# Kernel tuning notes

Measured on AMD Instinct MI355X. Metric: run time of the kernel, lower is better.

The kernel has to match this reference:

```python
import jax, jax.numpy as jnp
import numpy as np

N_NODES = 50000


def setup_inputs() -> dict:
    key = jax.random.key(0)
    k1, k2, k3, k4 = jax.random.split(key, 4)
    in_dim, out_dim, n_edges = 128, 64, 800000
    x = jax.random.normal(k1, (N_NODES, in_dim), dtype=jnp.float32)
    edge_index = jax.random.randint(k2, (2, n_edges), 0, N_NODES, dtype=jnp.int64)
    W = jax.random.normal(k3, (in_dim, out_dim), dtype=jnp.float32) * (1.0 / np.sqrt(in_dim))
    att = jax.random.normal(k4, (2 * out_dim,), dtype=jnp.float32) * (1.0 / np.sqrt(2 * out_dim))
    return {"x": x, "edge_index": edge_index, "W": W, "att": att}


def reference(x, edge_index, W, att):
    N = x.shape[0]
    F_out = W.shape[1]
    h = x @ W                                   # [N, F]
    src, dst = edge_index[0], edge_index[1]
    hs = h[src]                                 # [E, F] gather
    hd = h[dst]                                 # [E, F] gather
    # att(cat([h_src, h_dst])) == h_src @ a1 + h_dst @ a2
    a1, a2 = att[:F_out], att[F_out:]
    logit = jax.nn.leaky_relu(hs @ a1 + hd @ a2, 0.2)   # [E]
    E = logit.shape[0]
    # The original builds a dense [N, E] matrix (row d holds logit_e at col e
    # for dst[e]==d, zeros elsewhere) and softmaxes over the E axis. The
    # equivalent sparse form: denom_d = sum_{e:dst=d} exp(logit_e) + (E - deg_d)*exp(0),
    # stabilized with m_d = max(max logit over segment, 0).
    seg_max = jax.ops.segment_max(logit, dst, num_segments=N)      # -inf on empty
    m = jnp.maximum(seg_max, 0.0)                                  # include the zero cells
    exp_l = jnp.exp(logit - m[dst])                                # [E]
    seg_sum = jax.ops.segment_sum(exp_l, dst, num_segments=N)      # [N]
    deg = jax.ops.segment_sum(jnp.ones_like(logit), dst, num_segments=N)
    denom = seg_sum + (jnp.float32(E) - deg) * jnp.exp(-m)         # zeros' contribution
    w = exp_l / denom[dst]                                          # [E]
    agg = jax.ops.segment_sum(w[:, None] * hs, dst, num_segments=N)  # [N, F]
    return jax.nn.elu(agg)
```

## Files before the change

### kernel.cpp

```cpp
#include <hip/hip_runtime.h>
#include <hip/hip_bf16.h>

#define FIN 128
#define FOUT 64
#define BINW 128
#define NBINPAD 512
#define QS 2560
#define TILE 4096
#define DPQ 32
#define RCAP 768

typedef __attribute__((ext_vector_type(8))) short short8;
typedef __attribute__((ext_vector_type(4))) float f32x4;

__device__ __forceinline__ unsigned short f2bf(float f) {
    unsigned u = __float_as_uint(f);
    unsigned r = u + 0x7FFFu + ((u >> 16) & 1u);
    return (unsigned short)(r >> 16);
}

__device__ __forceinline__ float f16lo(unsigned u) {
    return (float)__builtin_bit_cast(_Float16, (unsigned short)(u & 0xFFFFu));
}
__device__ __forceinline__ float f16hi(unsigned u) {
    return (float)__builtin_bit_cast(_Float16, (unsigned short)(u >> 16));
}

__global__ __launch_bounds__(256) void k_prep(
    const float* __restrict__ W,
    unsigned short* __restrict__ Whig, unsigned short* __restrict__ Wlog,
    int* __restrict__ qcur, int nzero)
{
    const int t = threadIdx.x;
    if (blockIdx.x >= 64) {
        const int i = (blockIdx.x - 64) * 256 + t;
        if (i < nzero) qcur[i] = 0;
        return;
    }
    const int f = blockIdx.x * 256 + t;
    const int combo = f >> 9;
    const int s = combo >> 2, c = combo & 3;
    const int r = f & 511;
    const int l = r >> 3, j = r & 7;
    const int k = s * 32 + (l >> 4) * 8 + j;
    const int n = c * 16 + (l & 15);
    const float w = W[k * 64 + n];
    const unsigned short hi = f2bf(w);
    const float hif = __uint_as_float((unsigned)hi << 16);
    Whig[f] = hi;
    Wlog[f] = f2bf(w - hif);
}

__global__ __launch_bounds__(256, 8) void k_fused(
    const float* __restrict__ x, const unsigned short* __restrict__ Whig,
    const unsigned short* __restrict__ Wlog, const float* __restrict__ att,
    unsigned* __restrict__ h2, float* __restrict__ as_, float* __restrict__ ad_,
    const int* __restrict__ src, const int* __restrict__ dst,
    unsigned* __restrict__ queue, int* __restrict__ qcur,
    int N, int E, int nbins, int paBlocks)
{
    union SMem {
        struct { unsigned rec[TILE]; int hist[NBINPAD]; int scanb[NBINPAD];
                 int comb[NBINPAD]; } pa;
    };
    __shared__ SMem sm;
    const int t = threadIdx.x;

    if ((int)blockIdx.x < paBlocks) {
        const int e0 = blockIdx.x * TILE;
        const int tot = (E - e0 < TILE) ? (E - e0) : TILE;
        sm.pa.hist[t] = 0; sm.pa.hist[t + 256] = 0;
        __syncthreads();
        #pragma unroll
        for (int i = 0; i < TILE / 256; ++i) {
            const int e = e0 + i * 256 + t;
            if (e < E) atomicAdd(&sm.pa.hist[__builtin_nontemporal_load(dst + e) >> 7], 1);
        }
        __syncthreads();
        const int v0 = sm.pa.hist[t], v1 = sm.pa.hist[t + 256];
        sm.pa.scanb[t] = v0; sm.pa.scanb[t + 256] = v1;
        __syncthreads();
        #pragma unroll
        for (int off = 1; off < NBINPAD; off <<= 1) {
            const int a0 = (t >= off) ? sm.pa.scanb[t - off] : 0;
            const int a1 = (t + 256 >= off) ? sm.pa.scanb[t + 256 - off] : 0;
            __syncthreads();
            sm.pa.scanb[t] += a0; sm.pa.scanb[t + 256] += a1;
            __syncthreads();
        }
        const int ex0 = sm.pa.scanb[t] - v0;
        const int ex1 = sm.pa.scanb[t + 256] - v1;
        int c0 = 0, c1 = 0;
        if (t < nbins && v0 > 0)
            c0 = t * QS + atomicAdd(qcur + t, v0) - ex0;
        if (t + 256 < nbins && v1 > 0)
            c1 = (t + 256) * QS + atomicAdd(qcur + t + 256, v1) - ex1;
        sm.pa.hist[t] = ex0; sm.pa.hist[t + 256] = ex1;
        sm.pa.comb[t] = c0;  sm.pa.comb[t + 256] = c1;
        __syncthreads();
        #pragma unroll
        for (int i = 0; i < TILE / 256; ++i) {
            const int e = e0 + i * 256 + t;
            if (e < E) {
                const int d = __builtin_nontemporal_load(dst + e);
                const int s = __builtin_nontemporal_load(src + e);
                const int pos = atomicAdd(&sm.pa.hist[d >> 7], 1);
                sm.pa.rec[pos] = (unsigned)s | ((unsigned)d << 16);
            }
        }
        __syncthreads();
        for (int i = t; i < tot; i += 256) {
            const unsigned r = sm.pa.rec[i];
            const int b = (int)(r >> 23);
            const int gpos = sm.pa.comb[b] + i;
            if (gpos < (b + 1) * QS)
                __builtin_nontemporal_store(r, queue + gpos);
        }
        return;
    }

    const int bb = blockIdx.x - paBlocks;
    const int wv = t >> 6, lane = t & 63;
    const int quad = lane >> 4, mrow = lane & 15;
    const int r0 = (bb * 4 + wv) * 16;
    const int arow = r0 + mrow;
    const bool rok = arow < N;

    f32x4 acc[4] = {};

    #pragma unroll
    for (int s = 0; s < 4; ++s) {
        float xv[8];
        if (rok) {
            const float4* p = (const float4*)(x + (size_t)arow * FIN + s * 32 + quad * 8);
            const float4 u0 = p[0], u1 = p[1];
            xv[0] = u0.x; xv[1] = u0.y; xv[2] = u0.z; xv[3] = u0.w;
            xv[4] = u1.x; xv[5] = u1.y; xv[6] = u1.z; xv[7] = u1.w;
        } else {
            #pragma unroll
            for (int j = 0; j < 8; ++j) xv[j] = 0.f;
        }
        short8 ah, al;
        #pragma unroll
        for (int j = 0; j < 8; ++j) {
            const unsigned short hi = f2bf(xv[j]);
            const float hif = __uint_as_float((unsigned)hi << 16);
            ah[j] = (short)hi;
            al[j] = (short)f2bf(xv[j] - hif);
        }
        #pragma unroll
        for (int c = 0; c < 4; ++c) {
            const short8 bh = *(const short8*)&Whig[((s * 4 + c) * 64 + lane) * 8];
            const short8 bl = *(const short8*)&Wlog[((s * 4 + c) * 64 + lane) * 8];
            acc[c] = __builtin_amdgcn_mfma_f32_16x16x32_bf16(ah, bh, acc[c], 0, 0, 0);
            acc[c] = __builtin_amdgcn_mfma_f32_16x16x32_bf16(al, bh, acc[c], 0, 0, 0);
            acc[c] = __builtin_amdgcn_mfma_f32_16x16x32_bf16(ah, bl, acc[c], 0, 0, 0);
        }
    }

    float a1v[4], a2v[4];
    #pragma unroll
    for (int c = 0; c < 4; ++c) {
        a1v[c] = att[c * 16 + mrow];
        a2v[c] = att[64 + c * 16 + mrow];
    }
    #pragma unroll
    for (int reg = 0; reg < 4; ++reg) {
        float pa = 0.f, pb = 0.f;
        #pragma unroll
        for (int c = 0; c < 4; ++c) {
            pa = fmaf(acc[c][reg], a1v[c], pa);
            pb = fmaf(acc[c][reg], a2v[c], pb);
        }
        #pragma unroll
        for (int off = 1; off < 16; off <<= 1) {
            pa += __shfl_xor(pa, off);
            pb += __shfl_xor(pb, off);
        }
        const int orow = r0 + quad * 4 + reg;
        if (mrow == 0 && orow < N) {
            as_[orow] = pa;
            ad_[orow] = pb;
        }
    }

    #pragma unroll
    for (int reg = 0; reg < 4; ++reg) {
        const int orow = r0 + quad * 4 + reg;
        if (orow < N) {
            #pragma unroll
            for (int c = 0; c < 2; ++c) {
                const unsigned lo = (unsigned)__builtin_bit_cast(unsigned short,
                                        (_Float16)acc[c][reg]);
                const unsigned hi = (unsigned)__builtin_bit_cast(unsigned short,
                                        (_Float16)acc[c + 2][reg]);
                h2[(size_t)orow * 32 + c * 16 + mrow] = lo | (hi << 16);
            }
        }
    }
}

__global__ __launch_bounds__(256) void k_aggq(
    const int* __restrict__ qcur, const unsigned* __restrict__ queue,
    const float* __restrict__ as_, const float* __restrict__ ad_,
    const unsigned* __restrict__ h2, float* __restrict__ out,
    int N, float Ef)
{
    __shared__ unsigned rec[RCAP];
    __shared__ unsigned pay[RCAP];
    __shared__ float wexp[RCAP];
    __shared__ int hist[DPQ], base[DPQ], cur[DPQ];
    __shared__ float adl[DPQ];
    __shared__ int nloc;

    const int bin = blockIdx.x >> 2, q = blockIdx.x & 3;
    const int d0 = bin * BINW + q * DPQ;
    const int t = threadIdx.x;
    const int wv = t >> 6, lane = t & 63;

    if (t < DPQ) {
        hist[t] = 0;
        const int d = d0 + t;
        adl[t] = (d < N) ? ad_[d] : 0.f;
    }
    if (t == 0) nloc = 0;
    __syncthreads();

    int cnt = qcur[bin];
    if (cnt > QS) cnt = QS;

    for (int i = t; i < cnt; i += 256) {
        const unsigned r = __builtin_nontemporal_load(queue + (size_t)bin * QS + i);
        const bool m = ((int)((r >> 21) & 3) == q);
        const unsigned long long mk = __ballot(m);
        int b0 = 0;
        if (lane == 0 && mk) b0 = atomicAdd(&nloc, __popcll(mk));
        b0 = __shfl(b0, 0);
        if (m) {
            const int p = b0 + __popcll(mk & ((1ull << lane) - 1ull));
            if (p < RCAP) {
                rec[p] = r;
                atomicAdd(&hist[(r >> 16) & (DPQ - 1)], 1);
            }
        }
    }
    __syncthreads();
    int n = nloc; if (n > RCAP) n = RCAP;

    if (t < DPQ) base[t] = hist[t];
    __syncthreads();
    #pragma unroll
    for (int off = 1; off < DPQ; off <<= 1) {
        const int a = (t < DPQ && t >= off) ? base[t - off] : 0;
        __syncthreads();
        if (t < DPQ) base[t] += a;
        __syncthreads();
    }
    if (t < DPQ) { base[t] -= hist[t]; cur[t] = base[t]; }
    __syncthreads();

    for (int i = t; i < n; i += 256) {
        const unsigned r = rec[i];
        const int s  = (int)(r & 0xFFFFu);
        const int dl = (int)(r >> 16) & (DPQ - 1);
        const float z = as_[s] + adl[dl];
        const float lg = (z >= 0.f) ? z : 0.2f * z;
        const int pos = atomicAdd(&cur[dl], 1);
        pay[pos] = (unsigned)s;
        wexp[pos] = expf(lg);
    }
    __syncthreads();

    const int grp = lane >> 4, ln = lane & 15;
    const int g16 = wv * 4 + grp;
    #pragma unroll
    for (int k = 0; k < 2; ++k) {
        const int dl = g16 + k * 16;
        const int d = d0 + dl;
        const bool ok = (d < N);
        const int dg = ok ? hist[dl] : 0;
        const int bs = ok ? base[dl] : 0;

        float ss = 0.f;
        for (int j = ln; j < dg; j += 16) ss += wexp[bs + j];
        ss += __shfl_xor(ss, 8, 16);
        ss += __shfl_xor(ss, 4, 16);
        ss += __shfl_xor(ss, 2, 16);
        ss += __shfl_xor(ss, 1, 16);
        const float inv = 1.f / (ss + (Ef - (float)dg));

        float a00 = 0.f, a01 = 0.f, a10 = 0.f, a11 = 0.f;
        for (int jb = 0; jb < dg; jb += 8) {
            float w[8]; int s[8];
            #pragma unroll
            for (int u = 0; u < 8; ++u) {
                const int j = jb + u;
                if (j < dg) {
                    s[u] = (int)pay[bs + j];
                    w[u] = wexp[bs + j] * inv;
                } else { s[u] = 0; w[u] = 0.f; }
            }
            #pragma unroll
            for (int u = 0; u < 8; ++u) {
                const uint2 hp = *(const uint2*)&h2[(size_t)s[u] * 32 + 2 * ln];
                a00 += w[u] * f16lo(hp.x);
                a01 += w[u] * f16hi(hp.x);
                a10 += w[u] * f16lo(hp.y);
                a11 += w[u] * f16hi(hp.y);
            }
        }

        if (ok) {
            const float r00 = (a00 > 0.f) ? a00 : expm1f(a00);
            const float r10 = (a10 > 0.f) ? a10 : expm1f(a10);
            const float r01 = (a01 > 0.f) ? a01 : expm1f(a01);
            const float r11 = (a11 > 0.f) ? a11 : expm1f(a11);
            float2* op0 = (float2*)(out + (size_t)d * FOUT + 2 * ln);
            float2* op1 = (float2*)(out + (size_t)d * FOUT + 32 + 2 * ln);
            *op0 = make_float2(r00, r10);
            *op1 = make_float2(r01, r11);
        }
    }
}

extern "C" void kernel_launch(void* const* d_in, const int* in_sizes, int n_in,
                              void* d_out, int out_size, void* d_ws, size_t ws_size,
                              hipStream_t stream) {
    const float* x   = (const float*)d_in[0];
    const int*   ei  = (const int*)d_in[1];
    const float* W   = (const float*)d_in[2];
    const float* att = (const float*)d_in[3];

    const int N = in_sizes[0] / FIN;
    const int E = in_sizes[1] / 2;
    const int* src = ei;
    const int* dst = ei + E;

    const int NBINS = (N + BINW - 1) / BINW;

    char* ws = (char*)d_ws;
    size_t o = 0;
    auto carve = [&](size_t bytes) {
        void* p = ws + o; o += (bytes + 1023) & ~(size_t)1023; return p;
    };
    unsigned short* Whig = (unsigned short*)carve(16384 * 2);
    unsigned short* Wlog = (unsigned short*)carve(16384 * 2);
    float*          as_  = (float*)carve((size_t)N * 4);
    float*          ad_  = (float*)carve((size_t)N * 4);
    int*            qcur = (int*)carve((size_t)NBINS * 4);
    unsigned*       h2   = (unsigned*)carve((size_t)N * 32 * 4);
    unsigned*       queue = (unsigned*)carve((size_t)NBINS * QS * 4);

    float* out = (float*)d_out;

    const int paBlocks = (E + TILE - 1) / TILE;
    const int mmBlocks = (N + 63) / 64;
    const int zBlks    = (NBINS + 255) / 256;

    k_prep<<<64 + zBlks, 256, 0, stream>>>(W, Whig, Wlog, qcur, NBINS);
    k_fused<<<paBlocks + mmBlocks, 256, 0, stream>>>(
        x, Whig, Wlog, att, h2, as_, ad_, src, dst, queue, qcur, N, E, NBINS, paBlocks);
    k_aggq<<<NBINS * 4, 256, 0, stream>>>(qcur, queue, as_, ad_, h2, out, N, (float)E);
}
```

Before: 127.8 us.

## Replace shared-memory Hillis-Steele scan with wave shuffle scan and single edge read

The edge-binning phase now reads src/dst once, staging packed records in LDS while building the histogram, instead of reading dst twice from global memory. The 512-bin exclusive scan moves from a barrier-heavy LDS Hillis-Steele scan (two syncs per step) to a per-wave shuffle scan plus a small cross-wave combine. Scatter positions are now assigned with per-bin LDS atomics during the global write rather than through a separate sorted LDS pass. The cost is that output order within a bin becomes nondeterministic and global stores are less contiguous than the previously sorted layout.

```diff
diff --git a/kernel.cpp b/kernel.cpp
--- a/kernel.cpp
+++ b/kernel.cpp
@@ -60,8 +60,8 @@
     int N, int E, int nbins, int paBlocks)
 {
     union SMem {
-        struct { unsigned rec[TILE]; int hist[NBINPAD]; int scanb[NBINPAD];
-                 int comb[NBINPAD]; } pa;
+        struct { unsigned rec[TILE]; int hist[NBINPAD]; int comb[NBINPAD];
+                 int wtot[4]; } pa;
     };
     __shared__ SMem sm;
     const int t = threadIdx.x;
@@ -69,52 +69,56 @@
     if ((int)blockIdx.x < paBlocks) {
         const int e0 = blockIdx.x * TILE;
         const int tot = (E - e0 < TILE) ? (E - e0) : TILE;
+        const int wv = t >> 6, lane = t & 63;
         sm.pa.hist[t] = 0; sm.pa.hist[t + 256] = 0;
         __syncthreads();
         #pragma unroll
         for (int i = 0; i < TILE / 256; ++i) {
-            const int e = e0 + i * 256 + t;
-            if (e < E) atomicAdd(&sm.pa.hist[__builtin_nontemporal_load(dst + e) >> 7], 1);
-        }
-        __syncthreads();
-        const int v0 = sm.pa.hist[t], v1 = sm.pa.hist[t + 256];
-        sm.pa.scanb[t] = v0; sm.pa.scanb[t + 256] = v1;
-        __syncthreads();
-        #pragma unroll
-        for (int off = 1; off < NBINPAD; off <<= 1) {
-            const int a0 = (t >= off) ? sm.pa.scanb[t - off] : 0;
-            const int a1 = (t + 256 >= off) ? sm.pa.scanb[t + 256 - off] : 0;
-            __syncthreads();
-            sm.pa.scanb[t] += a0; sm.pa.scanb[t + 256] += a1;
-            __syncthreads();
-        }
-        const int ex0 = sm.pa.scanb[t] - v0;
-        const int ex1 = sm.pa.scanb[t + 256] - v1;
-        int c0 = 0, c1 = 0;
-        if (t < nbins && v0 > 0)
-            c0 = t * QS + atomicAdd(qcur + t, v0) - ex0;
-        if (t + 256 < nbins && v1 > 0)
-            c1 = (t + 256) * QS + atomicAdd(qcur + t + 256, v1) - ex1;
-        sm.pa.hist[t] = ex0; sm.pa.hist[t + 256] = ex1;
-        sm.pa.comb[t] = c0;  sm.pa.comb[t + 256] = c1;
-        __syncthreads();
-        #pragma unroll
-        for (int i = 0; i < TILE / 256; ++i) {
-            const int e = e0 + i * 256 + t;
+            const int idx = i * 256 + t;
+            const int e = e0 + idx;
             if (e < E) {
                 const int d = __builtin_nontemporal_load(dst + e);
                 const int s = __builtin_nontemporal_load(src + e);
-                const int pos = atomicAdd(&sm.pa.hist[d >> 7], 1);
-                sm.pa.rec[pos] = (unsigned)s | ((unsigned)d << 16);
-            }
-        }
-        __syncthreads();
-        for (int i = t; i < tot; i += 256) {
-            const unsigned r = sm.pa.rec[i];
-            const int b = (int)(r >> 23);
-            const int gpos = sm.pa.comb[b] + i;
-            if (gpos < (b + 1) * QS)
-                __builtin_nontemporal_store(r, queue + gpos);
+                sm.pa.rec[idx] = (unsigned)s | ((unsigned)d << 16);
+                atomicAdd(&sm.pa.hist[d >> 7], 1);
+            }
+        }
+        __syncthreads();
+        const int b0 = 2 * t;
+        const int v0 = sm.pa.hist[b0], v1 = sm.pa.hist[b0 + 1];
+        const int tv = v0 + v1;
+        int sc = tv;
+        #pragma unroll
+        for (int off = 1; off < 64; off <<= 1) {
+            const int nb = __shfl_up(sc, off);
+            if (lane >= off) sc += nb;
+        }
+        if (lane == 63) sm.pa.wtot[wv] = sc;
+        __syncthreads();
+        int wbase = 0;
+        #pragma unroll
+        for (int w = 0; w < 4; ++w) wbase += (w < wv) ? sm.pa.wtot[w] : 0;
+        const int ex0 = wbase + (sc - tv);
+        const int ex1 = ex0 + v0;
+        int c0 = 0, c1 = 0;
+        if (b0 < nbins && v0 > 0)
+            c0 = b0 * QS + atomicAdd(qcur + b0, v0) - ex0;
+        if (b0 + 1 < nbins && v1 > 0)
+            c1 = (b0 + 1) * QS + atomicAdd(qcur + b0 + 1, v1) - ex1;
+        sm.pa.hist[b0] = ex0; sm.pa.hist[b0 + 1] = ex1;
+        sm.pa.comb[b0] = c0;  sm.pa.comb[b0 + 1] = c1;
+        __syncthreads();
+        #pragma unroll
+        for (int i = 0; i < TILE / 256; ++i) {
+            const int idx = i * 256 + t;
+            if (idx < tot) {
+                const unsigned r = sm.pa.rec[idx];
+                const int b = (int)(r >> 23);
+                const int pos = atomicAdd(&sm.pa.hist[b], 1);
+                const int gpos = sm.pa.comb[b] + pos;
+                if (gpos < (b + 1) * QS)
+                    __builtin_nontemporal_store(r, queue + gpos);
+            }
         }
         return;
     }
```

Result: slower. 141.9 us (+11.0%).
